# Performance work log

Measured on AMD Instinct MI355X. Metric: run time of the kernel, lower is better.

Reference implementation:

```python
import jax, jax.numpy as jnp
import numpy as np

# ---- dimensions ----
N = 16384      # nodes
E = 131072     # edges (avg degree 8)
F = 128        # scalar channel width == s_dim
L = 9          # spherical-harmonic components (lmax=2)
R = 8          # radial basis size
DOUT = L * F   # post-product node width (1152)
K = 1024       # fixed number of master nodes (static stand-in for m>0.5)
HID = 64       # master-selection hidden dim
DA = 64        # virtual-attention head dim
LAMBDA_ATTN = 0.5
R_CUT = 5.0
EPS = 1e-9


def sh_l2(u):
    # real SH polynomials up to l=2 on unit vectors u[..., 3] -> [..., 9]
    x, y, z = u[..., 0], u[..., 1], u[..., 2]
    o = jnp.ones_like(x)
    return jnp.stack([o, x, y, z, x * y, y * z, 3.0 * z * z - 1.0, x * z, x * x - y * y], axis=-1)


def bessel(r):
    # Bessel radial basis; r [..., 1] -> [..., R]
    n = jnp.arange(1, R + 1, dtype=r.dtype)
    return jnp.sqrt(2.0 / R_CUT) * jnp.sin(n * jnp.pi * r / R_CUT) / jnp.maximum(r, EPS)


def setup_inputs() -> dict:
    key = jax.random.key(0)
    ks = jax.random.split(key, 18)
    s = lambda d: 1.0 / np.sqrt(d)
    return {
        'h': jax.random.normal(ks[0], (N, F), jnp.float32),
        'pos': 3.0 * jax.random.normal(ks[1], (N, 3), jnp.float32),
        'edge_sh': jax.random.normal(ks[2], (E, L), jnp.float32),
        'edge_feats': jax.random.uniform(ks[3], (E, R), jnp.float32),
        'W_node_l': s(F) * jax.random.normal(ks[4], (F, F), jnp.float32),
        'W_rad_l': s(R) * jax.random.normal(ks[5], (R, F), jnp.float32),
        'W_prod_l': s(L * F) * jax.random.normal(ks[6], (L, F, DOUT), jnp.float32),
        'ms_W1': s(F) * jax.random.normal(ks[7], (F, HID), jnp.float32),
        'ms_b1': jnp.zeros((HID,), jnp.float32),
        'ms_W2': s(HID) * jax.random.normal(ks[8], (HID, 1), jnp.float32),
        'ms_b2': jnp.zeros((1,), jnp.float32),
        'vg_Wq': s(F) * jax.random.normal(ks[9], (F, DA), jnp.float32),
        'vg_Wk': s(F) * jax.random.normal(ks[10], (F, DA), jnp.float32),
        'W_node_h': s(DOUT) * jax.random.normal(ks[11], (DOUT, F), jnp.float32),
        'W_rad_h': s(R) * jax.random.normal(ks[12], (R, F), jnp.float32),
        'W_prod_h': s(L * F) * jax.random.normal(ks[13], (L, F, DOUT), jnp.float32),
        'edge_index': jax.random.randint(ks[14], (2, E), 0, N),
    }


def reference(h, pos, edge_sh, edge_feats, W_node_l, W_rad_l, W_prod_l,
              ms_W1, ms_b1, ms_W2, ms_b2, vg_Wq, vg_Wk,
              W_node_h, W_rad_h, W_prod_h, edge_index):
    src, dst = edge_index[0], edge_index[1]

    # ---- local conv + reshape + prod (with padded residual sc) ----
    t = (h[src] @ W_node_l) * (edge_feats @ W_rad_l)                      # [E,F]
    msg = edge_sh[:, :, None] * t[:, None, :]                             # [E,L,F]
    upd = jax.ops.segment_sum(msg, dst, num_segments=N)                   # [N,L,F]
    sc = jnp.pad(h, ((0, 0), (0, DOUT - F)))
    h_local = jnp.einsum('nlf,lfg->ng', upd, W_prod_l) + sc               # [N,DOUT]

    # ---- master selection (MLP -> sigmoid); fixed top-K masters ----
    hs = h_local[:, :F]
    m = jax.nn.sigmoid(jax.nn.relu(hs @ ms_W1 + ms_b1) @ ms_W2 + ms_b2)[:, 0]  # [N]
    _, midx = jax.lax.top_k(m, K)
    master_idx = jnp.sort(midx)                                           # [K]

    # ---- induced subgraph among masters as dense [K,K] adjacency ----
    rank = jnp.full((N,), K, dtype=jnp.int32).at[master_idx].set(jnp.arange(K, dtype=jnp.int32))
    adj = jnp.zeros((K + 1, K + 1), h.dtype).at[rank[src], rank[dst]].max(jnp.ones((E,), h.dtype))
    adj_induced = adj[:K, :K]

    h_m = h_local[master_idx]                                             # [K,DOUT]
    pos_m = pos[master_idx]                                               # [K,3]
    hms = h_m[:, :F]

    # ---- virtual graph generation (attention -> thresholded dense adj) ----
    q = hms @ vg_Wq
    kk = hms @ vg_Wk
    A = jax.nn.sigmoid(q @ kk.T / jnp.sqrt(jnp.asarray(DA, h.dtype)))     # [K,K]
    A_virtual = jnp.where(A > LAMBDA_ATTN, A, 0.0)
    eye = jnp.eye(K, dtype=bool)
    Bv = (A_virtual > 0) & ~eye                                           # remove self loops
    Bv = Bv | Bv.T                                                        # to_undirected
    adj_master = jnp.clip(adj_induced + Bv.astype(h.dtype), 0.0, 1.0) * (1.0 - jnp.eye(K, dtype=h.dtype))

    # ---- hierarchical conv over dense master graph ----
    A_rec = adj_master.T                                                  # A_rec[i,j]=1: sender j -> receiver i
    V = pos_m[None, :, :] - pos_m[:, None, :]                             # vec = pos[src]-pos[dst]
    r = jnp.linalg.norm(V, axis=-1, keepdims=True)                        # [K,K,1]
    u = V / jnp.maximum(r, EPS)
    sh_m = sh_l2(u)                                                       # [K,K,L]
    rad = bessel(r)                                                       # [K,K,R]
    tm = (h_m @ W_node_h)[None, :, :] * (rad @ W_rad_h) * A_rec[:, :, None]  # [K,K,F]
    upd_m = jnp.einsum('ijl,ijf->ilf', sh_m, tm)                          # [K,L,F]
    h_hier = jnp.einsum('ilf,lfg->ig', upd_m, W_prod_h) + h_m             # sc_master pad is 0-width

    # ---- masked scatter blend ----
    h_exp = jnp.zeros_like(h_local).at[master_idx].set(h_hier)
    h_final = (1.0 - m[:, None]) * h_local + m[:, None] * h_exp
    return (h_final, A_virtual, m, master_idx)
```

## Files before the change

kernel.cpp:

```cpp
#include <hip/hip_runtime.h>
#include <hip/hip_bf16.h>
#include <stdint.h>

#define N_NODES 16384
#define E_EDGES 131072
#define F_DIM 128
#define L_DIM 9
#define R_DIM 8
#define DOUT_DIM 1152
#define K_SEL 1024
#define HID_DIM 64
#define DA_DIM 64

typedef unsigned short u16;
typedef __attribute__((ext_vector_type(8))) short bf16x8;
typedef __attribute__((ext_vector_type(4))) float f32x4;

static __device__ inline u16 f2bs(float x) {
  union { __hip_bfloat16 b; u16 s; } u;
  u.b = __float2bfloat16(x);
  return u.s;
}

#define GLDS16(gsrc, ldst) __builtin_amdgcn_global_load_lds( \
    (__attribute__((address_space(1))) void*)(void*)(gsrc),  \
    (__attribute__((address_space(3))) void*)(ldst), 16, 0, 0)

__global__ __launch_bounds__(256) void gemm_mfma(
    const float* __restrict__ A, const u16* __restrict__ Bt,
    float* __restrict__ C, int ldc, int M, int Nc, int Kc,
    const float* __restrict__ Add, int ldadd, int addW)
{
  __shared__ float Af[128 * 32];
  __shared__ u16  Bs[128 * 32];
  const int tid = threadIdx.x;
  const int wave = tid >> 6, lane = tid & 63;
  const int wm = wave >> 1, wn = wave & 1;
  const int l15 = lane & 15, quad = lane >> 4;
  const int bm = blockIdx.y * 128, bn = blockIdx.x * 128;

  f32x4 acc[4][4];
#pragma unroll
  for (int i = 0; i < 4; i++)
#pragma unroll
    for (int j = 0; j < 4; j++) acc[i][j] = (f32x4)(0.f);

  for (int k0 = 0; k0 < Kc; k0 += 32) {
    __syncthreads();
#pragma unroll
    for (int it = 0; it < 4; it++) {
      int c = it * 256 + tid;
      int row = c >> 3, op = c & 7;
      int oct = op ^ (row & 7);
      const float* g = A + (size_t)(bm + row) * Kc + k0 + oct * 4;
      GLDS16(g, &Af[c * 4]);
    }
#pragma unroll
    for (int it = 0; it < 2; it++) {
      int c = it * 256 + tid;
      int row = c >> 2, qp = c & 3;
      int q = qp ^ ((row >> 1) & 3);
      const u16* g = Bt + (size_t)(bn + row) * Kc + k0 + q * 8;
      GLDS16(g, &Bs[c * 8]);
    }
    __syncthreads();

    bf16x8 af[4], bfg[4];
#pragma unroll
    for (int mi = 0; mi < 4; mi++) {
      int m = wm * 64 + mi * 16 + l15;
      int o0 = (quad * 2) ^ (m & 7), o1 = (quad * 2 + 1) ^ (m & 7);
      float4 lo = *(const float4*)&Af[m * 32 + o0 * 4];
      float4 hi = *(const float4*)&Af[m * 32 + o1 * 4];
      bf16x8 r;
      r[0] = (short)f2bs(lo.x); r[1] = (short)f2bs(lo.y);
      r[2] = (short)f2bs(lo.z); r[3] = (short)f2bs(lo.w);
      r[4] = (short)f2bs(hi.x); r[5] = (short)f2bs(hi.y);
      r[6] = (short)f2bs(hi.z); r[7] = (short)f2bs(hi.w);
      af[mi] = r;
    }
#pragma unroll
    for (int ni = 0; ni < 4; ni++) {
      int n = wn * 64 + ni * 16 + l15;
      int q2 = quad ^ ((n >> 1) & 3);
      bfg[ni] = *(const bf16x8*)&Bs[n * 32 + q2 * 8];
    }
#pragma unroll
    for (int mi = 0; mi < 4; mi++)
#pragma unroll
      for (int ni = 0; ni < 4; ni++)
        acc[mi][ni] = __builtin_amdgcn_mfma_f32_16x16x32_bf16(af[mi], bfg[ni], acc[mi][ni], 0, 0, 0);
  }
#pragma unroll
  for (int mi = 0; mi < 4; mi++)
#pragma unroll
    for (int ni = 0; ni < 4; ni++)
#pragma unroll
      for (int r = 0; r < 4; r++) {
        int row = bm + wm * 64 + mi * 16 + quad * 4 + r;
        int col = bn + wn * 64 + ni * 16 + l15;
        float v = acc[mi][ni][r];
        if (Add != nullptr && col < addW) v += Add[(size_t)row * ldadd + col];
        C[(size_t)row * ldc + col] = v;
      }
}

__global__ __launch_bounds__(256) void transpose_bf16(
    const float* __restrict__ W, u16* __restrict__ Bt, int K, int N)
{
  __shared__ float t[32][33];
  const int n0 = blockIdx.x * 32, k0 = blockIdx.y * 32;
  const int tx = threadIdx.x & 31, ty = threadIdx.x >> 5;
  for (int r = ty; r < 32; r += 8) t[r][tx] = W[(size_t)(k0 + r) * N + n0 + tx];
  __syncthreads();
  for (int r = ty; r < 32; r += 8) Bt[(size_t)(n0 + r) * K + k0 + tx] = f2bs(t[tx][r]);
}

#define BM 128
#define BN 128
#define BK 16
__global__ __launch_bounds__(256) void gemm_f32(
    const float* __restrict__ A, int lda,
    const float* __restrict__ B, int ldb,
    float* __restrict__ C, int ldc,
    int M, int Nc, int Kc,
    const float* __restrict__ Add, int ldadd, int addW)
{
  __shared__ float As[BK][BM + 1];
  __shared__ float Bs[BK][BN];
  const int tid = threadIdx.x;
  const int tx = tid & 15, ty = tid >> 4;
  const int bm = blockIdx.y * BM, bn = blockIdx.x * BN;
  float acc[8][8];
#pragma unroll
  for (int i = 0; i < 8; i++)
#pragma unroll
    for (int j = 0; j < 8; j++) acc[i][j] = 0.f;
  for (int k0 = 0; k0 < Kc; k0 += BK) {
    const int ac = tid & 15, ar0 = tid >> 4;
#pragma unroll
    for (int rr = 0; rr < 8; rr++) {
      int row = ar0 + rr * 16;
      As[ac][row] = A[(size_t)(bm + row) * lda + k0 + ac];
    }
    const int bc = tid & 127, br0 = tid >> 7;
#pragma unroll
    for (int rr = 0; rr < 8; rr++) {
      int kr = br0 + rr * 2;
      Bs[kr][bc] = B[(size_t)(k0 + kr) * ldb + bn + bc];
    }
    __syncthreads();
#pragma unroll
    for (int kk = 0; kk < BK; kk++) {
      float a[8], b[8];
#pragma unroll
      for (int i = 0; i < 8; i++) a[i] = As[kk][ty * 8 + i];
#pragma unroll
      for (int j = 0; j < 8; j++) b[j] = Bs[kk][tx * 8 + j];
#pragma unroll
      for (int i = 0; i < 8; i++)
#pragma unroll
        for (int j = 0; j < 8; j++) acc[i][j] = fmaf(a[i], b[j], acc[i][j]);
    }
    __syncthreads();
  }
#pragma unroll
  for (int i = 0; i < 8; i++) {
    int row = bm + ty * 8 + i;
#pragma unroll
    for (int j = 0; j < 8; j++) {
      int col = bn + tx * 8 + j;
      float v = acc[i][j];
      if (Add != nullptr && col < addW) v += Add[(size_t)row * ldadd + col];
      C[(size_t)row * ldc + col] = v;
    }
  }
}

__global__ __launch_bounds__(256) void gemm64_f32(
    const float* __restrict__ A, int lda,
    const float* __restrict__ B, int ldb,
    float* __restrict__ C, int ldc,
    int M, int Nc, int Kc, int kPerSplit,
    const float* __restrict__ Add, int ldadd, int addW)
{
  __shared__ float As[16][65];
  __shared__ float Bs[16][64];
  const int tid = threadIdx.x;
  const int tx = tid & 15, ty = tid >> 4;
  const int bm = blockIdx.y * 64, bn = blockIdx.x * 64;
  const int kb = blockIdx.z * kPerSplit;
  const int ke = min(kb + kPerSplit, Kc);
  float acc[4][4];
#pragma unroll
  for (int i = 0; i < 4; i++)
#pragma unroll
    for (int j = 0; j < 4; j++) acc[i][j] = 0.f;
  for (int k0 = kb; k0 < ke; k0 += 16) {
    const int ac = tid & 15, ar = tid >> 4;
#pragma unroll
    for (int rr = 0; rr < 4; rr++) {
      int row = ar + rr * 16;
      As[ac][row] = A[(size_t)(bm + row) * lda + k0 + ac];
    }
    const int bc = tid & 63, br = tid >> 6;
#pragma unroll
    for (int rr = 0; rr < 4; rr++) {
      int kr = br + rr * 4;
      Bs[kr][bc] = B[(size_t)(k0 + kr) * ldb + bn + bc];
    }
    __syncthreads();
#pragma unroll
    for (int kk = 0; kk < 16; kk++) {
      float a[4], b[4];
#pragma unroll
      for (int i = 0; i < 4; i++) a[i] = As[kk][ty * 4 + i];
#pragma unroll
      for (int j = 0; j < 4; j++) b[j] = Bs[kk][tx * 4 + j];
#pragma unroll
      for (int i = 0; i < 4; i++)
#pragma unroll
        for (int j = 0; j < 4; j++) acc[i][j] = fmaf(a[i], b[j], acc[i][j]);
    }
    __syncthreads();
  }
#pragma unroll
  for (int i = 0; i < 4; i++) {
    int row = bm + ty * 4 + i;
#pragma unroll
    for (int j = 0; j < 4; j++) {
      int col = bn + tx * 4 + j;
      if (gridDim.z > 1) {
        atomicAdd(&C[(size_t)row * ldc + col], acc[i][j]);
      } else {
        float v = acc[i][j];
        if (Add != nullptr && col < addW) v += Add[(size_t)row * ldadd + col];
        C[(size_t)row * ldc + col] = v;
      }
    }
  }
}

__global__ __launch_bounds__(256) void count_kernel(
    const int* __restrict__ ei, int* __restrict__ counts)
{
  int e = blockIdx.x * 256 + threadIdx.x;
  atomicAdd(&counts[ei[E_EDGES + e]], 1);
}

__global__ __launch_bounds__(1024) void scan_kernel(
    const int* __restrict__ counts, int* __restrict__ offsets, int* __restrict__ cursor)
{
  __shared__ int part[1024];
  const int t = threadIdx.x;
  const int base = t * 16;
  int loc[16];
  int s = 0;
#pragma unroll
  for (int k = 0; k < 16; k++) { loc[k] = counts[base + k]; s += loc[k]; }
  part[t] = s;
  __syncthreads();
  for (int d = 1; d < 1024; d <<= 1) {
    int v = (t >= d) ? part[t - d] : 0;
    __syncthreads();
    part[t] += v;
    __syncthreads();
  }
  int run = part[t] - s;
#pragma unroll
  for (int k = 0; k < 16; k++) {
    offsets[base + k] = run;
    cursor[base + k] = run;
    run += loc[k];
  }
}

__global__ __launch_bounds__(256) void fill_kernel(
    const int* __restrict__ ei, int* __restrict__ cursor, int* __restrict__ elist)
{
  int e = blockIdx.x * 256 + threadIdx.x;
  int d = ei[E_EDGES + e];
  int p = atomicAdd(&cursor[d], 1);
  elist[p] = e;
}

__global__ __launch_bounds__(128) void gather_accum_kernel(
    const float* __restrict__ hW, const float* __restrict__ edge_sh,
    const float* __restrict__ edge_feats, const float* __restrict__ W_rad_l,
    const int* __restrict__ ei, const int* __restrict__ offsets,
    const int* __restrict__ counts, const int* __restrict__ elist,
    float* __restrict__ upd)
{
  __shared__ float sWr[R_DIM * F_DIM];
  const int d = blockIdx.x, f = threadIdx.x;
  for (int t = f; t < R_DIM * F_DIM; t += 128) sWr[t] = W_rad_l[t];
  __syncthreads();
  const int b = offsets[d], n = counts[d];
  float acc[L_DIM];
#pragma unroll
  for (int l = 0; l < L_DIM; l++) acc[l] = 0.f;
  for (int k = 0; k < n; k++) {
    const int e = elist[b + k];
    const int s = ei[e];
    float rw = 0.f;
#pragma unroll
    for (int p = 0; p < R_DIM; p++)
      rw = fmaf(edge_feats[(size_t)e * R_DIM + p], sWr[p * F_DIM + f], rw);
    const float tf = hW[(size_t)s * F_DIM + f] * rw;
#pragma unroll
    for (int l = 0; l < L_DIM; l++)
      acc[l] = fmaf(edge_sh[(size_t)e * L_DIM + l], tf, acc[l]);
  }
#pragma unroll
  for (int l = 0; l < L_DIM; l++)
    upd[(size_t)d * DOUT_DIM + l * F_DIM + f] = acc[l];
}

__global__ __launch_bounds__(256) void gate_kernel(
    const float* __restrict__ hs, const float* __restrict__ W1,
    const float* __restrict__ b1, const float* __restrict__ W2,
    const float* __restrict__ b2, float* __restrict__ m_ws, float* __restrict__ m_out,
    int* __restrict__ hist1)
{
  __shared__ float sW1[F_DIM * HID_DIM];
  __shared__ float srow[4][F_DIM];
  const int tid = threadIdx.x;
  for (int t = tid; t < F_DIM * HID_DIM; t += 256) sW1[t] = W1[t];
  const int wave = tid >> 6, lane = tid & 63;
  const int n = blockIdx.x * 4 + wave;
  srow[wave][lane] = hs[(size_t)n * F_DIM + lane];
  srow[wave][lane + 64] = hs[(size_t)n * F_DIM + lane + 64];
  __syncthreads();
  float hid = b1[lane];
#pragma unroll 8
  for (int c = 0; c < F_DIM; c++) hid = fmaf(srow[wave][c], sW1[c * HID_DIM + lane], hid);
  hid = fmaxf(hid, 0.f);
  float v = hid * W2[lane];
#pragma unroll
  for (int off = 32; off > 0; off >>= 1) v += __shfl_down(v, off);
  if (lane == 0) {
    float mm = 1.f / (1.f + expf(-(v + b2[0])));
    m_ws[n] = mm;
    m_out[n] = mm;
    unsigned mb = __float_as_uint(mm);
    atomicAdd(&hist1[mb >> 16], 1);
  }
}

__global__ __launch_bounds__(1024) void radix_sel_kernel(
    const int* __restrict__ hist, const int* __restrict__ kin, int kinIdx,
    int* __restrict__ outp, int outIdx)
{
  __shared__ int part[1024];
  const int t = threadIdx.x;
  const int Kv = kin ? kin[kinIdx] : K_SEL;
  const int base = t * 64;
  int s = 0;
  for (int k = 0; k < 64; k++) s += hist[base + k];
  part[t] = s;
  __syncthreads();
  for (int d = 1; d < 1024; d <<= 1) {
    int v = (t + d < 1024) ? part[t + d] : 0;
    __syncthreads();
    part[t] += v;
    __syncthreads();
  }
  int inc = part[t];
  if (inc >= Kv && inc - s < Kv) {
    int r = inc - s;
    for (int b = base + 63; b >= base; b--) {
      int hv = hist[b];
      if (r + hv >= Kv) { outp[outIdx] = b; outp[outIdx + 1] = Kv - r; break; }
      r += hv;
    }
  }
}

__global__ __launch_bounds__(256) void hist2_kernel(
    const float* __restrict__ m_ws, const int* __restrict__ selb, int* __restrict__ hist2)
{
  int i = blockIdx.x * 256 + threadIdx.x;
  unsigned mb = __float_as_uint(m_ws[i]);
  if ((int)(mb >> 16) == selb[0]) atomicAdd(&hist2[mb & 0xFFFFu], 1);
}

__global__ __launch_bounds__(256) void flag_kernel(
    const float* __restrict__ m_ws, int* __restrict__ selb,
    unsigned char* __restrict__ flags, int* __restrict__ cand)
{
  int i = blockIdx.x * 256 + threadIdx.x;
  unsigned mb = __float_as_uint(m_ws[i]);
  unsigned vb = ((unsigned)selb[0] << 16) | (unsigned)selb[2];
  unsigned char fl = 0;
  if (mb > vb) fl = 1;
  else if (mb == vb) { int p = atomicAdd(&selb[4], 1); cand[p] = i; }
  flags[i] = fl;
}

__global__ __launch_bounds__(1024) void cand_kernel(
    const int* __restrict__ selb, const int* __restrict__ cand, unsigned char* __restrict__ flags)
{
  const int nc = selb[4], need = selb[3];
  for (int c = threadIdx.x; c < nc; c += 1024) {
    const int idx = cand[c];
    int r = 0;
    for (int o = 0; o < nc; o++) r += (cand[o] < idx) ? 1 : 0;
    if (r < need) flags[idx] = 1;
  }
}

__global__ __launch_bounds__(1024) void compact_kernel(
    const unsigned char* __restrict__ flags, int* __restrict__ midx,
    int* __restrict__ rank, float* __restrict__ mi_out)
{
  __shared__ int part[1024];
  const int t = threadIdx.x;
  const int base = t * 16;
  int loc[16];
  int s = 0;
#pragma unroll
  for (int k = 0; k < 16; k++) { loc[k] = flags[base + k]; s += loc[k]; }
  part[t] = s;
  __syncthreads();
  for (int d = 1; d < 1024; d <<= 1) {
    int v = (t >= d) ? part[t - d] : 0;
    __syncthreads();
    part[t] += v;
    __syncthreads();
  }
  int run = part[t] - s;
#pragma unroll
  for (int k = 0; k < 16; k++) {
    int i = base + k;
    if (loc[k]) {
      midx[run] = i;
      mi_out[run] = (float)i;
      rank[i] = run;
      run++;
    } else {
      rank[i] = K_SEL;
    }
  }
}

__global__ __launch_bounds__(256) void adj_kernel(
    const int* __restrict__ ei, const int* __restrict__ rank, unsigned char* __restrict__ adjm)
{
  int e = blockIdx.x * 256 + threadIdx.x;
  int rs = rank[ei[e]];
  int rd = rank[ei[E_EDGES + e]];
  if (rs < K_SEL && rd < K_SEL) adjm[(size_t)rs * K_SEL + rd] = 1;
}

__global__ __launch_bounds__(128) void gather_kernel(
    const float* __restrict__ hl, const float* __restrict__ pos,
    const int* __restrict__ midx, float* __restrict__ h_m, float* __restrict__ pos_m)
{
  const int rI = blockIdx.x, t = threadIdx.x;
  const int mi = midx[rI];
  for (int c = t; c < DOUT_DIM; c += 128)
    h_m[(size_t)rI * DOUT_DIM + c] = hl[(size_t)mi * DOUT_DIM + c];
  if (t < 3) pos_m[rI * 3 + t] = pos[mi * 3 + t];
}

__global__ __launch_bounds__(128) void qk_kernel(
    const float* __restrict__ hs, const int* __restrict__ midx,
    const float* __restrict__ Wq, const float* __restrict__ Wk,
    float* __restrict__ q, float* __restrict__ kk)
{
  __shared__ float row[F_DIM];
  const int i = blockIdx.x, t = threadIdx.x;
  const int mi = midx[i];
  row[t] = hs[(size_t)mi * F_DIM + t];
  __syncthreads();
  const int d = t & 63;
  const float* W = (t < 64) ? Wq : Wk;
  float acc = 0.f;
#pragma unroll 8
  for (int c = 0; c < F_DIM; c++) acc = fmaf(row[c], W[c * DA_DIM + d], acc);
  float* dst = (t < 64) ? q : kk;
  dst[(size_t)i * DA_DIM + d] = acc;
}

__global__ __launch_bounds__(256) void attn_kernel(
    const float* __restrict__ q, const float* __restrict__ kk,
    unsigned char* __restrict__ maskA, float* __restrict__ Av)
{
  __shared__ float qs[16][DA_DIM], ks[16][DA_DIM];
  const int tx = threadIdx.x, ty = threadIdx.y;
  const int tid = ty * 16 + tx;
  const int i0 = blockIdx.y * 16, j0 = blockIdx.x * 16;
  for (int t = tid; t < 16 * DA_DIM; t += 256) {
    int rr = t >> 6, cc = t & 63;
    qs[rr][cc] = q[(size_t)(i0 + rr) * DA_DIM + cc];
    ks[rr][cc] = kk[(size_t)(j0 + rr) * DA_DIM + cc];
  }
  __syncthreads();
  float acc = 0.f;
#pragma unroll
  for (int d2 = 0; d2 < DA_DIM; d2++) acc = fmaf(qs[ty][d2], ks[tx][d2], acc);
  float sgl = 1.f / (1.f + expf(-acc * 0.125f));
  size_t o = (size_t)(i0 + ty) * K_SEL + (j0 + tx);
  bool big = sgl > 0.5f;
  maskA[o] = big ? 1 : 0;
  Av[o] = big ? sgl : 0.f;
}

__global__ __launch_bounds__(256) void listbuild_kernel(
    const unsigned char* __restrict__ adjm, const unsigned char* __restrict__ maskA,
    u16* __restrict__ list, int* __restrict__ nj)
{
  __shared__ int cnt;
  const int i = blockIdx.x, tid = threadIdx.x;
  if (tid == 0) cnt = 0;
  __syncthreads();
#pragma unroll
  for (int jt = 0; jt < 4; jt++) {
    int j = jt * 256 + tid;
    bool e = (j != i) && (adjm[(size_t)j * K_SEL + i] | maskA[(size_t)j * K_SEL + i] |
                          maskA[(size_t)i * K_SEL + j]);
    if (e) {
      int p = atomicAdd(&cnt, 1);
      list[(size_t)i * K_SEL + p] = (u16)j;
    }
  }
  __syncthreads();
  if (tid == 0) nj[i] = cnt;
}

__global__ __launch_bounds__(512) void hier2_kernel(
    const float* __restrict__ hWn, const float* __restrict__ pos_m,
    const float* __restrict__ W_rad_h, const u16* __restrict__ list,
    const int* __restrict__ nj, float* __restrict__ upd_m)
{
  __shared__ float sW[R_DIM * F_DIM];
  __shared__ float gsm[128][20];
  __shared__ int sj[128];
  __shared__ float red[3][L_DIM][F_DIM];
  const int tid = threadIdx.x;
  const int i = blockIdx.x;
  const int f = tid & 127, jsub = tid >> 7;
  for (int t = tid; t < R_DIM * F_DIM; t += 512) sW[t] = W_rad_h[t];
  const float pix = pos_m[i * 3 + 0], piy = pos_m[i * 3 + 1], piz = pos_m[i * 3 + 2];
  float acc[L_DIM];
#pragma unroll
  for (int l = 0; l < L_DIM; l++) acc[l] = 0.f;
  const int n = nj[i];
  for (int c0 = 0; c0 < n; c0 += 128) {
    const int cnt = min(128, n - c0);
    __syncthreads();
    if (tid < cnt) {
      const int j = list[(size_t)i * K_SEL + c0 + tid];
      sj[tid] = j;
      float vx = pos_m[j * 3 + 0] - pix;
      float vy = pos_m[j * 3 + 1] - piy;
      float vz = pos_m[j * 3 + 2] - piz;
      float r = sqrtf(vx * vx + vy * vy + vz * vz);
      float rm = fmaxf(r, 1e-9f);
      float inv = 1.f / rm;
      float ux = vx * inv, uy = vy * inv, uz = vz * inv;
      gsm[tid][0] = 1.f; gsm[tid][1] = ux; gsm[tid][2] = uy; gsm[tid][3] = uz;
      gsm[tid][4] = ux * uy; gsm[tid][5] = uy * uz;
      gsm[tid][6] = 3.f * uz * uz - 1.f;
      gsm[tid][7] = ux * uz; gsm[tid][8] = ux * ux - uy * uy;
      float theta = 0.62831853071795864769f * r;
      float s1 = sinf(theta), c1 = cosf(theta);
      float coef = 0.632455532033675866f * inv;
      float snm2 = 0.f, snm1 = s1;
      gsm[tid][9] = s1 * coef;
#pragma unroll
      for (int nn = 2; nn <= R_DIM; nn++) {
        float sn = 2.f * c1 * snm1 - snm2;
        gsm[tid][8 + nn] = sn * coef;
        snm2 = snm1; snm1 = sn;
      }
      gsm[tid][17] = 0.f; gsm[tid][18] = 0.f; gsm[tid][19] = 0.f;
    }
    __syncthreads();
    for (int t = jsub; t < cnt; t += 4) {
      const int j = sj[t];
      const float hw = hWn[(size_t)j * F_DIM + f];
      float4 g0 = *(const float4*)&gsm[t][0];
      float4 g1 = *(const float4*)&gsm[t][4];
      float4 g2 = *(const float4*)&gsm[t][8];
      float4 g3 = *(const float4*)&gsm[t][12];
      float  g4 = gsm[t][16];
      float rw = g2.y * sW[0 * F_DIM + f];
      rw = fmaf(g2.z, sW[1 * F_DIM + f], rw);
      rw = fmaf(g2.w, sW[2 * F_DIM + f], rw);
      rw = fmaf(g3.x, sW[3 * F_DIM + f], rw);
      rw = fmaf(g3.y, sW[4 * F_DIM + f], rw);
      rw = fmaf(g3.z, sW[5 * F_DIM + f], rw);
      rw = fmaf(g3.w, sW[6 * F_DIM + f], rw);
      rw = fmaf(g4,   sW[7 * F_DIM + f], rw);
      const float tm = hw * rw;
      acc[0] = fmaf(g0.x, tm, acc[0]); acc[1] = fmaf(g0.y, tm, acc[1]);
      acc[2] = fmaf(g0.z, tm, acc[2]); acc[3] = fmaf(g0.w, tm, acc[3]);
      acc[4] = fmaf(g1.x, tm, acc[4]); acc[5] = fmaf(g1.y, tm, acc[5]);
      acc[6] = fmaf(g1.z, tm, acc[6]); acc[7] = fmaf(g1.w, tm, acc[7]);
      acc[8] = fmaf(g2.x, tm, acc[8]);
    }
  }
  __syncthreads();
  if (jsub > 0) {
#pragma unroll
    for (int l = 0; l < L_DIM; l++) red[jsub - 1][l][f] = acc[l];
  }
  __syncthreads();
  if (jsub == 0) {
#pragma unroll
    for (int l = 0; l < L_DIM; l++) {
      float v = acc[l] + red[0][l][f] + red[1][l][f] + red[2][l][f];
      upd_m[(size_t)i * DOUT_DIM + l * F_DIM + f] = v;
    }
  }
}

__global__ __launch_bounds__(256) void combine_kernel(
    float* __restrict__ out0, const float* __restrict__ h_hier,
    const float* __restrict__ m_ws, const int* __restrict__ rank)
{
  size_t idx = (size_t)blockIdx.x * 256 + threadIdx.x;
  int n = (int)(idx / DOUT_DIM);
  int g = (int)(idx % DOUT_DIM);
  float mv = m_ws[n];
  float hl = out0[idx];
  int r = rank[n];
  float he = (r < K_SEL) ? h_hier[(size_t)r * DOUT_DIM + g] : 0.f;
  out0[idx] = (1.f - mv) * hl + mv * he;
}

extern "C" void kernel_launch(void* const* d_in, const int* in_sizes, int n_in,
                              void* d_out, int out_size, void* d_ws, size_t ws_size,
                              hipStream_t stream)
{
  const float* h         = (const float*)d_in[0];
  const float* pos       = (const float*)d_in[1];
  const float* edge_sh   = (const float*)d_in[2];
  const float* edge_feats= (const float*)d_in[3];
  const float* W_node_l  = (const float*)d_in[4];
  const float* W_rad_l   = (const float*)d_in[5];
  const float* W_prod_l  = (const float*)d_in[6];
  const float* ms_W1     = (const float*)d_in[7];
  const float* ms_b1     = (const float*)d_in[8];
  const float* ms_W2     = (const float*)d_in[9];
  const float* ms_b2     = (const float*)d_in[10];
  const float* vg_Wq     = (const float*)d_in[11];
  const float* vg_Wk     = (const float*)d_in[12];
  const float* W_node_h  = (const float*)d_in[13];
  const float* W_rad_h   = (const float*)d_in[14];
  const float* W_prod_h  = (const float*)d_in[15];
  const int*   eidx      = (const int*)d_in[16];

  float* out    = (float*)d_out;
  float* out_hf = out;
  float* out_Av = out + (size_t)N_NODES * DOUT_DIM;
  float* out_m  = out_Av + (size_t)K_SEL * K_SEL;
  float* out_mi = out_m + N_NODES;

  char* ws = (char*)d_ws;
  float* upd = (float*)ws;
  float* hW  = (float*)(ws + (size_t)N_NODES * DOUT_DIM * 4);
  float* hs  = hW;
  u16* Btl = (u16*)out_Av;
  char* csr = (char*)out_Av + (((size_t)DOUT_DIM * DOUT_DIM * 2 + 255) & ~(size_t)255);
  int* counts  = (int*)csr;
  int* offsets = counts + N_NODES;
  int* cursor  = offsets + N_NODES;
  int* elist   = cursor + N_NODES;
  size_t off = 0;
  auto alloc = [&](size_t bytes) -> void* {
    void* p = ws + off;
    off += (bytes + 255) & ~(size_t)255;
    return p;
  };
  float* m_ws  = (float*)alloc((size_t)N_NODES * 4);
  int*   rank  = (int*)alloc((size_t)N_NODES * 4);
  int*   midx  = (int*)alloc((size_t)K_SEL * 4);
  int*   hist1 = (int*)alloc((size_t)65536 * 4);
  int*   hist2 = (int*)alloc((size_t)65536 * 4);
  int*   selb  = (int*)alloc((size_t)64 * 4);
  int*   cand  = (int*)alloc((size_t)N_NODES * 4);
  unsigned char* flags = (unsigned char*)alloc((size_t)N_NODES);
  unsigned char* adjm  = (unsigned char*)alloc((size_t)K_SEL * K_SEL);
  unsigned char* maskA = (unsigned char*)alloc((size_t)K_SEL * K_SEL);
  float* qbuf  = (float*)alloc((size_t)K_SEL * DA_DIM * 4);
  float* kbuf  = (float*)alloc((size_t)K_SEL * DA_DIM * 4);
  float* h_m   = (float*)alloc((size_t)K_SEL * DOUT_DIM * 4);
  float* pos_m = (float*)alloc((size_t)K_SEL * 3 * 4);
  float* hWn   = (float*)alloc((size_t)K_SEL * F_DIM * 4);
  float* upd_m = (float*)alloc((size_t)K_SEL * DOUT_DIM * 4);
  float* h_hier= (float*)alloc((size_t)K_SEL * DOUT_DIM * 4);
  u16*   Bth   = (u16*)alloc((size_t)DOUT_DIM * DOUT_DIM * 2);
  u16*   jlist = (u16*)alloc((size_t)K_SEL * K_SEL * 2);
  int*   njbuf = (int*)alloc((size_t)K_SEL * 4);

  hipMemsetAsync(counts, 0, (size_t)N_NODES * 4, stream);
  transpose_bf16<<<dim3(DOUT_DIM / 32, DOUT_DIM / 32), 256, 0, stream>>>(
      W_prod_l, Btl, DOUT_DIM, DOUT_DIM);
  gemm_f32<<<dim3(1, N_NODES / 128), 256, 0, stream>>>(
      h, F_DIM, W_node_l, F_DIM, hW, F_DIM, N_NODES, F_DIM, F_DIM, nullptr, 0, 0);
  count_kernel<<<E_EDGES / 256, 256, 0, stream>>>(eidx, counts);
  scan_kernel<<<1, 1024, 0, stream>>>(counts, offsets, cursor);
  fill_kernel<<<E_EDGES / 256, 256, 0, stream>>>(eidx, cursor, elist);
  gather_accum_kernel<<<N_NODES, 128, 0, stream>>>(
      hW, edge_sh, edge_feats, W_rad_l, eidx, offsets, counts, elist, upd);
  gemm64_f32<<<dim3(F_DIM / 64, N_NODES / 64, 1), 256, 0, stream>>>(
      upd, DOUT_DIM, W_prod_l, DOUT_DIM, hs, F_DIM,
      N_NODES, F_DIM, DOUT_DIM, DOUT_DIM, h, F_DIM, F_DIM);
  gemm_mfma<<<dim3(DOUT_DIM / 128, N_NODES / 128), 256, 0, stream>>>(
      upd, Btl, out_hf, DOUT_DIM, N_NODES, DOUT_DIM, DOUT_DIM, h, F_DIM, F_DIM);

  hipMemsetAsync(adjm, 0, (size_t)K_SEL * K_SEL, stream);
  hipMemsetAsync(hist1, 0, (size_t)65536 * 4 * 2 + 256, stream);
  transpose_bf16<<<dim3(DOUT_DIM / 32, DOUT_DIM / 32), 256, 0, stream>>>(
      W_prod_h, Bth, DOUT_DIM, DOUT_DIM);
  gate_kernel<<<N_NODES / 4, 256, 0, stream>>>(hs, ms_W1, ms_b1, ms_W2, ms_b2,
                                               m_ws, out_m, hist1);
  radix_sel_kernel<<<1, 1024, 0, stream>>>(hist1, nullptr, 0, selb, 0);
  hist2_kernel<<<N_NODES / 256, 256, 0, stream>>>(m_ws, selb, hist2);
  radix_sel_kernel<<<1, 1024, 0, stream>>>(hist2, selb, 1, selb, 2);
  flag_kernel<<<N_NODES / 256, 256, 0, stream>>>(m_ws, selb, flags, cand);
  cand_kernel<<<1, 1024, 0, stream>>>(selb, cand, flags);
  compact_kernel<<<1, 1024, 0, stream>>>(flags, midx, rank, out_mi);
  adj_kernel<<<E_EDGES / 256, 256, 0, stream>>>(eidx, rank, adjm);
  gather_kernel<<<K_SEL, 128, 0, stream>>>(out_hf, pos, midx, h_m, pos_m);
  qk_kernel<<<K_SEL, 128, 0, stream>>>(hs, midx, vg_Wq, vg_Wk, qbuf, kbuf);
  attn_kernel<<<dim3(K_SEL / 16, K_SEL / 16), dim3(16, 16), 0, stream>>>(qbuf, kbuf, maskA, out_Av);
  listbuild_kernel<<<K_SEL, 256, 0, stream>>>(adjm, maskA, jlist, njbuf);
  hipMemsetAsync(hWn, 0, (size_t)K_SEL * F_DIM * 4, stream);
  gemm64_f32<<<dim3(F_DIM / 64, K_SEL / 64, 4), 256, 0, stream>>>(
      h_m, DOUT_DIM, W_node_h, F_DIM, hWn, F_DIM,
      K_SEL, F_DIM, DOUT_DIM, DOUT_DIM / 4, nullptr, 0, 0);
  hier2_kernel<<<K_SEL, 512, 0, stream>>>(hWn, pos_m, W_rad_h, jlist, njbuf, upd_m);
  gemm_mfma<<<dim3(DOUT_DIM / 128, K_SEL / 128), 256, 0, stream>>>(
      upd_m, Bth, h_hier, DOUT_DIM, K_SEL, DOUT_DIM, DOUT_DIM, h_m, DOUT_DIM, DOUT_DIM);
  combine_kernel<<<(N_NODES * DOUT_DIM) / 256, 256, 0, stream>>>(out_hf, h_hier, m_ws, rank);
}
```

Measured before the change: 784.6 us.

## Emit bf16 activations upstream and feed MFMA GEMMs via direct LDS loads

The gather and hierarchical conv kernels now also write a bf16 copy of their update tensors. A new MFMA GEMM variant loads that bf16 data straight into LDS with swizzling and an XCD-aware block remap, instead of converting fp32 inside the GEMM. The gather and combine kernels are also vectorised to float4. This trades extra bf16 writes and workspace for less GEMM load and convert traffic, and falls back to the old path if the workspace is too small.

```diff
diff --git a/kernel.cpp b/kernel.cpp
--- a/kernel.cpp
+++ b/kernel.cpp
@@ -105,6 +105,78 @@
       }
 }
 
+__global__ __launch_bounds__(256) void gemm_mfma_b16(
+    const u16* __restrict__ A, const u16* __restrict__ Bt,
+    float* __restrict__ C, int ldc, int Kc, int nbx, int nwg,
+    const float* __restrict__ Add, int ldadd, int addW)
+{
+  __shared__ u16 As[128 * 32];
+  __shared__ u16 Bs[128 * 32];
+  const int tid = threadIdx.x;
+  const int wave = tid >> 6, lane = tid & 63;
+  const int wm = wave >> 1, wn = wave & 1;
+  const int l15 = lane & 15, quad = lane >> 4;
+  const int lin = blockIdx.x;
+  const int swz = (lin & 7) * (nwg >> 3) + (lin >> 3);
+  const int bm = (swz / nbx) * 128, bn = (swz % nbx) * 128;
+
+  f32x4 acc[4][4];
+#pragma unroll
+  for (int i = 0; i < 4; i++)
+#pragma unroll
+    for (int j = 0; j < 4; j++) acc[i][j] = (f32x4)(0.f);
+
+  for (int k0 = 0; k0 < Kc; k0 += 32) {
+    __syncthreads();
+#pragma unroll
+    for (int it = 0; it < 2; it++) {
+      int c = it * 256 + tid;
+      int row = c >> 2, qp = c & 3;
+      int q = qp ^ ((row >> 1) & 3);
+      const u16* g = A + (size_t)(bm + row) * Kc + k0 + q * 8;
+      GLDS16(g, &As[c * 8]);
+    }
+#pragma unroll
+    for (int it = 0; it < 2; it++) {
+      int c = it * 256 + tid;
+      int row = c >> 2, qp = c & 3;
+      int q = qp ^ ((row >> 1) & 3);
+      const u16* g = Bt + (size_t)(bn + row) * Kc + k0 + q * 8;
+      GLDS16(g, &Bs[c * 8]);
+    }
+    __syncthreads();
+
+    bf16x8 af[4], bfg[4];
+#pragma unroll
+    for (int mi = 0; mi < 4; mi++) {
+      int m = wm * 64 + mi * 16 + l15;
+      af[mi] = *(const bf16x8*)&As[m * 32 + (quad ^ ((m >> 1) & 3)) * 8];
+    }
+#pragma unroll
+    for (int ni = 0; ni < 4; ni++) {
+      int n = wn * 64 + ni * 16 + l15;
+      bfg[ni] = *(const bf16x8*)&Bs[n * 32 + (quad ^ ((n >> 1) & 3)) * 8];
+    }
+#pragma unroll
+    for (int mi = 0; mi < 4; mi++)
+#pragma unroll
+      for (int ni = 0; ni < 4; ni++)
+        acc[mi][ni] = __builtin_amdgcn_mfma_f32_16x16x32_bf16(af[mi], bfg[ni], acc[mi][ni], 0, 0, 0);
+  }
+#pragma unroll
+  for (int mi = 0; mi < 4; mi++)
+#pragma unroll
+    for (int ni = 0; ni < 4; ni++)
+#pragma unroll
+      for (int r = 0; r < 4; r++) {
+        int row = bm + wm * 64 + mi * 16 + quad * 4 + r;
+        int col = bn + wn * 64 + ni * 16 + l15;
+        float v = acc[mi][ni][r];
+        if (Add != nullptr && col < addW) v += Add[(size_t)row * ldadd + col];
+        C[(size_t)row * ldc + col] = v;
+      }
+}
+
 __global__ __launch_bounds__(256) void transpose_bf16(
     const float* __restrict__ W, u16* __restrict__ Bt, int K, int N)
 {
@@ -289,7 +361,7 @@
     const float* __restrict__ edge_feats, const float* __restrict__ W_rad_l,
     const int* __restrict__ ei, const int* __restrict__ offsets,
     const int* __restrict__ counts, const int* __restrict__ elist,
-    float* __restrict__ upd)
+    float* __restrict__ upd, u16* __restrict__ updb)
 {
   __shared__ float sWr[R_DIM * F_DIM];
   const int d = blockIdx.x, f = threadIdx.x;
@@ -314,6 +386,11 @@
 #pragma unroll
   for (int l = 0; l < L_DIM; l++)
     upd[(size_t)d * DOUT_DIM + l * F_DIM + f] = acc[l];
+  if (updb != nullptr) {
+#pragma unroll
+    for (int l = 0; l < L_DIM; l++)
+      updb[(size_t)d * DOUT_DIM + l * F_DIM + f] = f2bs(acc[l]);
+  }
 }
 
 __global__ __launch_bounds__(256) void gate_kernel(
@@ -458,8 +535,9 @@
 {
   const int rI = blockIdx.x, t = threadIdx.x;
   const int mi = midx[rI];
-  for (int c = t; c < DOUT_DIM; c += 128)
-    h_m[(size_t)rI * DOUT_DIM + c] = hl[(size_t)mi * DOUT_DIM + c];
+  const float4* src = (const float4*)(hl + (size_t)mi * DOUT_DIM);
+  float4* dst = (float4*)(h_m + (size_t)rI * DOUT_DIM);
+  for (int c = t; c < DOUT_DIM / 4; c += 128) dst[c] = src[c];
   if (t < 3) pos_m[rI * 3 + t] = pos[mi * 3 + t];
 }
 
@@ -531,7 +609,7 @@
 __global__ __launch_bounds__(512) void hier2_kernel(
     const float* __restrict__ hWn, const float* __restrict__ pos_m,
     const float* __restrict__ W_rad_h, const u16* __restrict__ list,
-    const int* __restrict__ nj, float* __restrict__ upd_m)
+    const int* __restrict__ nj, float* __restrict__ upd_m, u16* __restrict__ updb_m)
 {
   __shared__ float sW[R_DIM * F_DIM];
   __shared__ float gsm[128][20];
@@ -612,6 +690,7 @@
     for (int l = 0; l < L_DIM; l++) {
       float v = acc[l] + red[0][l][f] + red[1][l][f] + red[2][l][f];
       upd_m[(size_t)i * DOUT_DIM + l * F_DIM + f] = v;
+      updb_m[(size_t)i * DOUT_DIM + l * F_DIM + f] = f2bs(v);
     }
   }
 }
@@ -620,14 +699,20 @@
     float* __restrict__ out0, const float* __restrict__ h_hier,
     const float* __restrict__ m_ws, const int* __restrict__ rank)
 {
-  size_t idx = (size_t)blockIdx.x * 256 + threadIdx.x;
-  int n = (int)(idx / DOUT_DIM);
-  int g = (int)(idx % DOUT_DIM);
+  size_t i4 = (size_t)blockIdx.x * 256 + threadIdx.x;
+  int n = (int)(i4 / (DOUT_DIM / 4));
+  int g4 = (int)(i4 % (DOUT_DIM / 4));
   float mv = m_ws[n];
-  float hl = out0[idx];
   int r = rank[n];
-  float he = (r < K_SEL) ? h_hier[(size_t)r * DOUT_DIM + g] : 0.f;
-  out0[idx] = (1.f - mv) * hl + mv * he;
+  float4 hl = ((const float4*)out0)[i4];
+  float4 he = make_float4(0.f, 0.f, 0.f, 0.f);
+  if (r < K_SEL) he = ((const float4*)h_hier)[(size_t)r * (DOUT_DIM / 4) + g4];
+  float4 o;
+  o.x = (1.f - mv) * hl.x + mv * he.x;
+  o.y = (1.f - mv) * hl.y + mv * he.y;
+  o.z = (1.f - mv) * hl.z + mv * he.z;
+  o.w = (1.f - mv) * hl.w + mv * he.w;
+  ((float4*)out0)[i4] = o;
 }
 
 extern "C" void kernel_launch(void* const* d_in, const int* in_sizes, int n_in,
@@ -662,6 +747,10 @@
   float* upd = (float*)ws;
   float* hW  = (float*)(ws + (size_t)N_NODES * DOUT_DIM * 4);
   float* hs  = hW;
+  const size_t updbOff = (size_t)N_NODES * DOUT_DIM * 4 + (size_t)N_NODES * F_DIM * 4;
+  const size_t updbNeed = updbOff + (size_t)N_NODES * DOUT_DIM * 2;
+  const bool useB16 = (ws_size >= updbNeed);
+  u16* updb = (u16*)(ws + updbOff);
   u16* Btl = (u16*)out_Av;
   char* csr = (char*)out_Av + (((size_t)DOUT_DIM * DOUT_DIM * 2 + 255) & ~(size_t)255);
   int* counts  = (int*)csr;
@@ -694,6 +783,7 @@
   u16*   Bth   = (u16*)alloc((size_t)DOUT_DIM * DOUT_DIM * 2);
   u16*   jlist = (u16*)alloc((size_t)K_SEL * K_SEL * 2);
   int*   njbuf = (int*)alloc((size_t)K_SEL * 4);
+  u16*   updbm = (u16*)alloc((size_t)K_SEL * DOUT_DIM * 2);
 
   hipMemsetAsync(counts, 0, (size_t)N_NODES * 4, stream);
   transpose_bf16<<<dim3(DOUT_DIM / 32, DOUT_DIM / 32), 256, 0, stream>>>(
@@ -704,12 +794,19 @@
   scan_kernel<<<1, 1024, 0, stream>>>(counts, offsets, cursor);
   fill_kernel<<<E_EDGES / 256, 256, 0, stream>>>(eidx, cursor, elist);
   gather_accum_kernel<<<N_NODES, 128, 0, stream>>>(
-      hW, edge_sh, edge_feats, W_rad_l, eidx, offsets, counts, elist, upd);
+      hW, edge_sh, edge_feats, W_rad_l, eidx, offsets, counts, elist, upd,
+      useB16 ? updb : nullptr);
   gemm64_f32<<<dim3(F_DIM / 64, N_NODES / 64, 1), 256, 0, stream>>>(
       upd, DOUT_DIM, W_prod_l, DOUT_DIM, hs, F_DIM,
       N_NODES, F_DIM, DOUT_DIM, DOUT_DIM, h, F_DIM, F_DIM);
-  gemm_mfma<<<dim3(DOUT_DIM / 128, N_NODES / 128), 256, 0, stream>>>(
-      upd, Btl, out_hf, DOUT_DIM, N_NODES, DOUT_DIM, DOUT_DIM, h, F_DIM, F_DIM);
+  if (useB16) {
+    gemm_mfma_b16<<<(DOUT_DIM / 128) * (N_NODES / 128), 256, 0, stream>>>(
+        updb, Btl, out_hf, DOUT_DIM, DOUT_DIM, DOUT_DIM / 128,
+        (DOUT_DIM / 128) * (N_NODES / 128), h, F_DIM, F_DIM);
+  } else {
+    gemm_mfma<<<dim3(DOUT_DIM / 128, N_NODES / 128), 256, 0, stream>>>(
+        upd, Btl, out_hf, DOUT_DIM, N_NODES, DOUT_DIM, DOUT_DIM, h, F_DIM, F_DIM);
+  }
 
   hipMemsetAsync(adjm, 0, (size_t)K_SEL * K_SEL, stream);
   hipMemsetAsync(hist1, 0, (size_t)65536 * 4 * 2 + 256, stream);
@@ -732,8 +829,9 @@
   gemm64_f32<<<dim3(F_DIM / 64, K_SEL / 64, 4), 256, 0, stream>>>(
       h_m, DOUT_DIM, W_node_h, F_DIM, hWn, F_DIM,
       K_SEL, F_DIM, DOUT_DIM, DOUT_DIM / 4, nullptr, 0, 0);
-  hier2_kernel<<<K_SEL, 512, 0, stream>>>(hWn, pos_m, W_rad_h, jlist, njbuf, upd_m);
-  gemm_mfma<<<dim3(DOUT_DIM / 128, K_SEL / 128), 256, 0, stream>>>(
-      upd_m, Bth, h_hier, DOUT_DIM, K_SEL, DOUT_DIM, DOUT_DIM, h_m, DOUT_DIM, DOUT_DIM);
-  combine_kernel<<<(N_NODES * DOUT_DIM) / 256, 256, 0, stream>>>(out_hf, h_hier, m_ws, rank);
-}
+  hier2_kernel<<<K_SEL, 512, 0, stream>>>(hWn, pos_m, W_rad_h, jlist, njbuf, upd_m, updbm);
+  gemm_mfma_b16<<<(DOUT_DIM / 128) * (K_SEL / 128), 256, 0, stream>>>(
+      updbm, Bth, h_hier, DOUT_DIM, DOUT_DIM, DOUT_DIM / 128,
+      (DOUT_DIM / 128) * (K_SEL / 128), h_m, DOUT_DIM, DOUT_DIM);
+  combine_kernel<<<(N_NODES * DOUT_DIM / 4) / 256, 256, 0, stream>>>(out_hf, h_hier, m_ws, rank);
+}
```

New measurement: 734.2 us. -6.4%, faster.
